# Kernel optimization log

Hardware: AMD Instinct MI355X
Metric: run time of the kernel (lower is better)

## Reference

```python
import jax, jax.numpy as jnp
import numpy as np

C = 1024
H = 16
EPS = 1e-5

def _layernorm(x, g, b):
    mu = jnp.mean(x, axis=-1, keepdims=True)
    var = jnp.mean(jnp.square(x - mu), axis=-1, keepdims=True)
    return (x - mu) * jax.lax.rsqrt(var + EPS) * g + b

def _mha(xq, xkv, wq, bq, wk, bk, wv, bv, wo, bo, causal):
    B, T, Cm = xq.shape
    Tc = xkv.shape[1]
    d = Cm // H
    q = (xq @ wq + bq).reshape(B, T, H, d)
    k = (xkv @ wk + bk).reshape(B, Tc, H, d)
    v = (xkv @ wv + bv).reshape(B, Tc, H, d)
    att = jnp.einsum('bthd,bshd->bhts', q, k) * (1.0 / np.sqrt(d))
    if causal:
        mask = jnp.tril(jnp.ones((T, Tc), dtype=bool))
        att = jnp.where(mask[None, None], att, -jnp.inf)
    att = jax.nn.softmax(att, axis=-1)
    y = jnp.einsum('bhts,bshd->bthd', att, v).reshape(B, T, Cm)
    return y @ wo + bo


def setup_inputs() -> dict:
    key = jax.random.key(0)
    ks = jax.random.split(key, 20)
    s = 0.02
    w = lambda k: (s * jax.random.normal(k, (C, C))).astype(jnp.float32)
    inp = {
        'x': jax.random.normal(ks[0], (4, 1024, C), dtype=jnp.float32),
        'context': jax.random.normal(ks[1], (4, 1024, C), dtype=jnp.float32),
        'ln1_g': jnp.ones((C,)), 'ln1_b': jnp.zeros((C,)),
        'ln2_g': jnp.ones((C,)), 'ln2_b': jnp.zeros((C,)),
        'sa_wq': w(ks[2]), 'sa_bq': jnp.zeros((C,)),
        'sa_wk': w(ks[3]), 'sa_bk': jnp.zeros((C,)),
        'sa_wv': w(ks[4]), 'sa_bv': jnp.zeros((C,)),
        'sa_wo': w(ks[5]), 'sa_bo': jnp.zeros((C,)),
        'ca_wq': w(ks[6]), 'ca_bq': jnp.zeros((C,)),
        'ca_wk': w(ks[7]), 'ca_bk': jnp.zeros((C,)),
        'ca_wv': w(ks[8]), 'ca_bv': jnp.zeros((C,)),
        'ca_wo': w(ks[9]), 'ca_bo': jnp.zeros((C,)),
        'mlp_w1': (s * jax.random.normal(ks[10], (C, 4 * C))).astype(jnp.float32),
        'mlp_b1': jnp.zeros((4 * C,)),
        'mlp_w2': (s * jax.random.normal(ks[11], (4 * C, C))).astype(jnp.float32),
        'mlp_b2': jnp.zeros((C,)),
    }
    return inp


def reference(x, context, ln1_g, ln1_b, ln2_g, ln2_b,
              sa_wq, sa_bq, sa_wk, sa_bk, sa_wv, sa_bv, sa_wo, sa_bo,
              ca_wq, ca_bq, ca_wk, ca_bk, ca_wv, ca_bv, ca_wo, ca_bo,
              mlp_w1, mlp_b1, mlp_w2, mlp_b2):
    # x = x + self_attn(ln1(x))  (causal)
    x = x + _mha(_layernorm(x, ln1_g, ln1_b), _layernorm(x, ln1_g, ln1_b),
                 sa_wq, sa_bq, sa_wk, sa_bk, sa_wv, sa_bv, sa_wo, sa_bo, causal=True)
    # x = x + cross_attn(ln2(x), context)  (non-causal)
    x = x + _mha(_layernorm(x, ln2_g, ln2_b), context,
                 ca_wq, ca_bq, ca_wk, ca_bk, ca_wv, ca_bv, ca_wo, ca_bo, causal=False)
    # x = x + mlp(ln2(x))  -- note: the module reuses ln2 here (as in source)
    h = _layernorm(x, ln2_g, ln2_b)
    h = jax.nn.gelu(h @ mlp_w1 + mlp_b1, approximate=False) @ mlp_w2 + mlp_b2
    x = x + h
    return x
```

## Files before the change

### kernel.cpp

```cpp
#include <hip/hip_runtime.h>
#include <hip/hip_bf16.h>

typedef __attribute__((ext_vector_type(8))) short s8v;
typedef __attribute__((ext_vector_type(4))) float f4v;

#define DEV static __device__ __forceinline__

DEV unsigned short f2bf(float f) {
    unsigned int u = __builtin_bit_cast(unsigned int, f);
    unsigned int r = u + 0x7FFFu + ((u >> 16) & 1u);
    return (unsigned short)(r >> 16);
}

DEV f4v fzero() { f4v v = {0.f, 0.f, 0.f, 0.f}; return v; }

DEV float fgelu(float x) {
    float z = x * (1.5957691f + 0.07135482f * x * x);
    float s = __builtin_amdgcn_rcpf(1.0f + __expf(-z));
    return x * s;
}

DEV void gload16(const void* g, void* l) {
    __builtin_amdgcn_global_load_lds(
        (const __attribute__((address_space(1))) unsigned int*)g,
        (__attribute__((address_space(3))) unsigned int*)l, 16, 0, 0);
}

struct P8 { const float* p[8]; };
__global__ __launch_bounds__(256) void k_transpose8(
        P8 ws8, unsigned short* __restrict__ base) {
    __shared__ float tile[32][33];
    int z = blockIdx.z;
    const float* W = ws8.p[z];
    unsigned short* Wt = base + (size_t)z * 1024 * 1024;
    int tx = threadIdx.x & 31, ty = threadIdx.x >> 5;
    int n0 = blockIdx.x * 32, k0 = blockIdx.y * 32;
#pragma unroll
    for (int r = 0; r < 32; r += 8)
        tile[ty + r][tx] = W[(size_t)(k0 + ty + r) * 1024 + n0 + tx];
    __syncthreads();
#pragma unroll
    for (int r = 0; r < 32; r += 8)
        Wt[(size_t)(n0 + ty + r) * 1024 + k0 + tx] = f2bf(tile[tx][ty + r]);
}

__global__ __launch_bounds__(256) void k_transpose_bf16(
        const float* __restrict__ W, unsigned short* __restrict__ Wt, int K, int N) {
    __shared__ float tile[32][33];
    int tx = threadIdx.x & 31, ty = threadIdx.x >> 5;
    int n0 = blockIdx.x * 32, k0 = blockIdx.y * 32;
#pragma unroll
    for (int r = 0; r < 32; r += 8)
        tile[ty + r][tx] = W[(size_t)(k0 + ty + r) * N + n0 + tx];
    __syncthreads();
#pragma unroll
    for (int r = 0; r < 32; r += 8)
        Wt[(size_t)(n0 + ty + r) * K + k0 + tx] = f2bf(tile[tx][ty + r]);
}

__global__ __launch_bounds__(256) void k_f32_to_bf16(
        const float* __restrict__ in, unsigned short* __restrict__ out, int n) {
    int i = (blockIdx.x * 256 + threadIdx.x) * 8;
    if (i >= n) return;
    float4 a = *(const float4*)(in + i);
    float4 b = *(const float4*)(in + i + 4);
    uint4 o;
    o.x = f2bf(a.x) | ((unsigned)f2bf(a.y) << 16);
    o.y = f2bf(a.z) | ((unsigned)f2bf(a.w) << 16);
    o.z = f2bf(b.x) | ((unsigned)f2bf(b.y) << 16);
    o.w = f2bf(b.z) | ((unsigned)f2bf(b.w) << 16);
    *(uint4*)(out + i) = o;
}

__global__ __launch_bounds__(256) void k_bias_cat(
        const float* q, const float* k, const float* v,
        const float* k2, const float* v2, float* out) {
    int i = blockIdx.x * 256 + threadIdx.x;
    float val;
    if (i < 1024) val = q[i];
    else if (i < 2048) val = k[i - 1024];
    else if (i < 3072) val = v[i - 2048];
    else if (i < 4096) val = k2[i - 3072];
    else val = v2[i - 4096];
    out[i] = val;
}

__global__ __launch_bounds__(256) void k_layernorm(
        const float* __restrict__ x, const float* __restrict__ g,
        const float* __restrict__ b, unsigned short* __restrict__ out) {
    int row = blockIdx.x;
    int t = threadIdx.x;
    const float* xr = x + (size_t)row * 1024;
    float4 v = *(const float4*)(xr + t * 4);
    float s = v.x + v.y + v.z + v.w;
    float ss = v.x * v.x + v.y * v.y + v.z * v.z + v.w * v.w;
#pragma unroll
    for (int m = 1; m < 64; m <<= 1) { s += __shfl_xor(s, m); ss += __shfl_xor(ss, m); }
    __shared__ float red[16];
    int w = t >> 6;
    if ((t & 63) == 0) { red[w] = s; red[8 + w] = ss; }
    __syncthreads();
    s = red[0] + red[1] + red[2] + red[3];
    ss = red[8] + red[9] + red[10] + red[11];
    float mu = s * (1.f / 1024.f);
    float rstd = rsqrtf(ss * (1.f / 1024.f) - mu * mu + 1e-5f);
    float4 gv = *(const float4*)(g + t * 4);
    float4 bv = *(const float4*)(b + t * 4);
    float y0 = (v.x - mu) * rstd * gv.x + bv.x;
    float y1 = (v.y - mu) * rstd * gv.y + bv.y;
    float y2 = (v.z - mu) * rstd * gv.z + bv.z;
    float y3 = (v.w - mu) * rstd * gv.w + bv.w;
    uint2 o;
    o.x = f2bf(y0) | ((unsigned)f2bf(y1) << 16);
    o.y = f2bf(y2) | ((unsigned)f2bf(y3) << 16);
    *(uint2*)(out + (size_t)row * 1024 + t * 4) = o;
}

template <int EPI, int BM>
__global__ __launch_bounds__(256) void k_gemm(
        const unsigned short* __restrict__ A, const unsigned short* __restrict__ Bt,
        const float* __restrict__ bias, const float* __restrict__ res,
        void* __restrict__ outv, int M, int N, int K) {
    constexpr int WI = (BM == 128) ? 4 : 2;
    constexpr int ABUF = BM * 64;
    constexpr int BUFSZ = ABUF + 8192;
    __shared__ __align__(16) char smem[3 * BUFSZ];
    int nbx = N >> 7;
    int bid = blockIdx.x;
    int cpx = gridDim.x >> 3;
    int swz = (bid & 7) * cpx + (bid >> 3);
    int bx = swz % nbx, by = swz / nbx;
    int m0 = by * BM, n0 = bx << 7;
    int tid = threadIdx.x, w = tid >> 6, l = tid & 63;
    int wr = w >> 1, wc = w & 1;
    int lq = l >> 4, lc = l & 15;
    f4v acc[WI][4];
#pragma unroll
    for (int i = 0; i < WI; ++i)
#pragma unroll
        for (int j = 0; j < 4; ++j) acc[i][j] = fzero();
    const unsigned short* Ab = A + (size_t)m0 * K;
    const unsigned short* Bb = Bt + (size_t)n0 * K;
    int arow = w * 16 + (l >> 2);
    int ach = (((l & 3) ^ ((arow >> 1) & 3)) << 3);

    auto STAGE = [&](int t) {
        int kt = t << 5;
        char* buf = smem + (t % 3) * BUFSZ;
        gload16(Ab + (size_t)arow * K + kt + ach, buf + w * 1024);
        if constexpr (BM == 128)
            gload16(Ab + (size_t)(64 + arow) * K + kt + ach, buf + 4096 + w * 1024);
        gload16(Bb + (size_t)arow * K + kt + ach, buf + ABUF + w * 1024);
        gload16(Bb + (size_t)(64 + arow) * K + kt + ach, buf + ABUF + 4096 + w * 1024);
    };
    int cs = ((lq ^ ((lc >> 1) & 3)) << 4);
    auto COMPUTE = [&](int t) {
        const char* buf = smem + (t % 3) * BUFSZ;
        s8v af[WI], bfr[4];
#pragma unroll
        for (int i = 0; i < WI; ++i)
            af[i] = *(const s8v*)(buf + (wr * (BM / 2) + i * 16 + lc) * 64 + cs);
#pragma unroll
        for (int j = 0; j < 4; ++j)
            bfr[j] = *(const s8v*)(buf + ABUF + (wc * 64 + j * 16 + lc) * 64 + cs);
#pragma unroll
        for (int i = 0; i < WI; ++i)
#pragma unroll
            for (int j = 0; j < 4; ++j)
                acc[i][j] = __builtin_amdgcn_mfma_f32_16x16x32_bf16(af[i], bfr[j], acc[i][j], 0, 0, 0);
    };

    int NT = K >> 5;
    STAGE(0); STAGE(1);
    if constexpr (BM == 128) asm volatile("s_waitcnt vmcnt(4)" ::: "memory");
    else                     asm volatile("s_waitcnt vmcnt(3)" ::: "memory");
    __builtin_amdgcn_s_barrier();
    for (int t = 0; t < NT; ++t) {
        if (t + 2 < NT) STAGE(t + 2);
        COMPUTE(t);
        if (t + 2 < NT) {
            if constexpr (BM == 128) asm volatile("s_waitcnt vmcnt(4)" ::: "memory");
            else                     asm volatile("s_waitcnt vmcnt(3)" ::: "memory");
        } else if (t + 1 < NT) {
            asm volatile("s_waitcnt vmcnt(0)" ::: "memory");
        }
        __builtin_amdgcn_s_barrier();
    }

    float* esc = (float*)smem + w * 1088;
#pragma unroll
    for (int i = 0; i < WI; ++i) {
#pragma unroll
        for (int j = 0; j < 4; ++j)
#pragma unroll
            for (int r = 0; r < 4; ++r)
                esc[(lq * 4 + r) * 68 + j * 16 + lc] = acc[i][j][r];
#pragma unroll
        for (int p = 0; p < 4; ++p) {
            int rr = p * 4 + lq;
            float4 v = *(const float4*)(esc + rr * 68 + lc * 4);
            int row = m0 + wr * (BM / 2) + i * 16 + rr;
            int col = n0 + wc * 64 + lc * 4;
            float4 bv = *(const float4*)(bias + col);
            v.x += bv.x; v.y += bv.y; v.z += bv.z; v.w += bv.w;
            size_t idx = (size_t)row * N + col;
            if (EPI == 0) {
                ushort4 o;
                o.x = f2bf(v.x); o.y = f2bf(v.y); o.z = f2bf(v.z); o.w = f2bf(v.w);
                *(ushort4*)((unsigned short*)outv + idx) = o;
            } else if (EPI == 1) {
                ushort4 o;
                o.x = f2bf(fgelu(v.x)); o.y = f2bf(fgelu(v.y));
                o.z = f2bf(fgelu(v.z)); o.w = f2bf(fgelu(v.w));
                *(ushort4*)((unsigned short*)outv + idx) = o;
            } else {
                float4 rv = *(const float4*)(res + idx);
                v.x += rv.x; v.y += rv.y; v.z += rv.z; v.w += rv.w;
                *(float4*)((float*)outv + idx) = v;
            }
        }
    }
}

template <bool CAUSAL>
__global__ __launch_bounds__(256) void k_attn(
        const unsigned short* __restrict__ Q, int ldq,
        const unsigned short* __restrict__ Kp, int ldk,
        const unsigned short* __restrict__ Vp, int ldv,
        unsigned short* __restrict__ O, int ldo, int T) {
    __shared__ unsigned short Ks[64 * 64];
    __shared__ unsigned short Vt[64 * 64];
    __shared__ unsigned short Ps[4][16 * 64];
    int nqt = T >> 6;
    int qt0, qt1, bh;
    if (CAUSAL) {
        int pairs = nqt >> 1;
        int pr = blockIdx.x % pairs;
        bh = blockIdx.x / pairs;
        qt0 = pr; qt1 = nqt - 1 - pr;
    } else {
        qt1 = blockIdx.x % nqt;
        bh = blockIdx.x / nqt;
        qt0 = 0;
    }
    int b = bh >> 4, h = bh & 15;
    int tid = threadIdx.x, w = tid >> 6, l = tid & 63;
    int lq = l >> 4, lc = l & 15;
    size_t qoff = (size_t)b * T * ldq + h * 64;
    size_t koff = (size_t)b * T * ldk + h * 64;
    size_t voff = (size_t)b * T * ldv + h * 64;
    s8v qf1[2], qf0[2];
    {
        const unsigned short* qp = Q + qoff + (size_t)(qt1 * 64 + w * 16 + lc) * ldq + lq * 8;
        qf1[0] = *(const s8v*)qp;
        qf1[1] = *(const s8v*)(qp + 32);
        if (CAUSAL) {
            const unsigned short* q0p = Q + qoff + (size_t)(qt0 * 64 + w * 16 + lc) * ldq + lq * 8;
            qf0[0] = *(const s8v*)q0p;
            qf0[1] = *(const s8v*)(q0p + 32);
        }
    }
    s8v ones;
#pragma unroll
    for (int i = 0; i < 8; ++i) ones[i] = (short)0x3F80;
    f4v o1[4], o0[4];
    float m1r[4], l1r[4], m0r[4], l0r[4];
#pragma unroll
    for (int j = 0; j < 4; ++j) {
        o1[j] = fzero(); o0[j] = fzero();
        m1r[j] = -3.0e38f; l1r[j] = 0.f; m0r[j] = -3.0e38f; l0r[j] = 0.f;
    }
    int p = tid & 31, dbase = (tid >> 5) * 8;

    auto SMPV = [&](f4v (&sa)[4], f4v (&oa)[4], float (&mr)[4], float (&lr)[4],
                    int qt, int kt) {
        bool diag = CAUSAL && kt == qt;
#pragma unroll
        for (int j = 0; j < 4; ++j) {
            float pv[4];
            float tm = -3.0e38f;
#pragma unroll
            for (int jn = 0; jn < 4; ++jn) {
                float sv = sa[jn][j] * 0.125f;
                if (diag) {
                    int qg = w * 16 + lq * 4 + j;
                    int kg = jn * 16 + lc;
                    if (kg > qg) sv = -3.0e38f;
                }
                pv[jn] = sv;
                tm = fmaxf(tm, sv);
            }
#pragma unroll
            for (int m = 1; m < 16; m <<= 1) tm = fmaxf(tm, __shfl_xor(tm, m));
            float mnew = fmaxf(mr[j], tm);
            float alpha = __expf(mr[j] - mnew);
            mr[j] = mnew;
#pragma unroll
            for (int jn = 0; jn < 4; ++jn) {
                float e = __expf(pv[jn] - mnew);
                int colx = jn * 16 + lc, rowx = lq * 4 + j;
                *(unsigned short*)((char*)Ps[w] + rowx * 128 +
                                   ((((colx >> 3) ^ (rowx & 7)) << 4) | ((colx & 7) << 1))) = f2bf(e);
            }
            lr[j] *= alpha;
#pragma unroll
            for (int jn = 0; jn < 4; ++jn) oa[jn][j] *= alpha;
        }
        f4v sone = fzero();
#pragma unroll
        for (int kc = 0; kc < 2; ++kc) {
            s8v af = *(const s8v*)((const char*)Ps[w] + lc * 128 +
                                   (((kc * 4 + lq) ^ (lc & 7)) << 4));
            sone = __builtin_amdgcn_mfma_f32_16x16x32_bf16(af, ones, sone, 0, 0, 0);
#pragma unroll
            for (int jn = 0; jn < 4; ++jn) {
                int dd = jn * 16 + lc;
                s8v bf = *(const s8v*)((const char*)Vt + dd * 128 +
                                       (((kc * 4 + lq) ^ (dd & 7)) << 4));
                oa[jn] = __builtin_amdgcn_mfma_f32_16x16x32_bf16(af, bf, oa[jn], 0, 0, 0);
            }
        }
#pragma unroll
        for (int j = 0; j < 4; ++j) lr[j] += sone[j];
    };

    int ktend = CAUSAL ? (qt1 + 1) : nqt;
    for (int kt = 0; kt < ktend; ++kt) {
#pragma unroll
        for (int s = 0; s < 2; ++s) {
            int idx = s * 256 + w * 64 + l;
            int t = idx >> 3;
            int ch = (idx & 7) ^ (t & 7);
            gload16(Kp + koff + (size_t)(kt * 64 + t) * ldk + ch * 8,
                    (char*)Ks + s * 4096 + w * 1024);
        }
        {
            const unsigned short* vp = Vp + voff + (size_t)(kt * 64 + 2 * p) * ldv + dbase;
            s8v v0 = *(const s8v*)vp;
            s8v v1 = *(const s8v*)(vp + ldv);
#pragma unroll
            for (int j = 0; j < 8; ++j) {
                int dd = dbase + j;
                unsigned int val = (unsigned short)v0[j] | ((unsigned)(unsigned short)v1[j] << 16);
                *(unsigned int*)((char*)Vt + dd * 128 +
                                 ((((p >> 2) ^ (dd & 7)) << 4) | ((p & 3) << 2))) = val;
            }
        }
        __syncthreads();
        bool do0 = CAUSAL && (kt <= qt0);
        f4v sa1[4], sa0[4];
#pragma unroll
        for (int jn = 0; jn < 4; ++jn) {
            sa1[jn] = fzero();
            int t = jn * 16 + lc;
#pragma unroll
            for (int kc = 0; kc < 2; ++kc) {
                s8v bf = *(const s8v*)((const char*)Ks + t * 128 +
                                       (((kc * 4 + lq) ^ (t & 7)) << 4));
                sa1[jn] = __builtin_amdgcn_mfma_f32_16x16x32_bf16(qf1[kc], bf, sa1[jn], 0, 0, 0);
            }
        }
        if (do0) {
#pragma unroll
            for (int jn = 0; jn < 4; ++jn) {
                sa0[jn] = fzero();
                int t = jn * 16 + lc;
#pragma unroll
                for (int kc = 0; kc < 2; ++kc) {
                    s8v bf = *(const s8v*)((const char*)Ks + t * 128 +
                                           (((kc * 4 + lq) ^ (t & 7)) << 4));
                    sa0[jn] = __builtin_amdgcn_mfma_f32_16x16x32_bf16(qf0[kc], bf, sa0[jn], 0, 0, 0);
                }
            }
        }
        SMPV(sa1, o1, m1r, l1r, qt1, kt);
        if (do0) SMPV(sa0, o0, m0r, l0r, qt0, kt);
        __syncthreads();
    }
#pragma unroll
    for (int j = 0; j < 4; ++j) {
        float inv = 1.0f / l1r[j];
        int row = qt1 * 64 + w * 16 + lq * 4 + j;
#pragma unroll
        for (int jn = 0; jn < 4; ++jn)
            O[(size_t)(b * T + row) * ldo + h * 64 + jn * 16 + lc] = f2bf(o1[jn][j] * inv);
    }
    if (CAUSAL) {
#pragma unroll
        for (int j = 0; j < 4; ++j) {
            float inv = 1.0f / l0r[j];
            int row = qt0 * 64 + w * 16 + lq * 4 + j;
#pragma unroll
            for (int jn = 0; jn < 4; ++jn)
                O[(size_t)(b * T + row) * ldo + h * 64 + jn * 16 + lc] = f2bf(o0[jn][j] * inv);
        }
    }
}

extern "C" void kernel_launch(void* const* d_in, const int* in_sizes, int n_in,
                              void* d_out, int out_size, void* d_ws, size_t ws_size,
                              hipStream_t stream) {
    const float* x     = (const float*)d_in[0];
    const float* ctx   = (const float*)d_in[1];
    const float* ln1_g = (const float*)d_in[2];
    const float* ln1_b = (const float*)d_in[3];
    const float* ln2_g = (const float*)d_in[4];
    const float* ln2_b = (const float*)d_in[5];
    const float* sa_wq = (const float*)d_in[6];  const float* sa_bq = (const float*)d_in[7];
    const float* sa_wk = (const float*)d_in[8];  const float* sa_bk = (const float*)d_in[9];
    const float* sa_wv = (const float*)d_in[10]; const float* sa_bv = (const float*)d_in[11];
    const float* sa_wo = (const float*)d_in[12]; const float* sa_bo = (const float*)d_in[13];
    const float* ca_wq = (const float*)d_in[14]; const float* ca_bq = (const float*)d_in[15];
    const float* ca_wk = (const float*)d_in[16]; const float* ca_bk = (const float*)d_in[17];
    const float* ca_wv = (const float*)d_in[18]; const float* ca_bv = (const float*)d_in[19];
    const float* ca_wo = (const float*)d_in[20]; const float* ca_bo = (const float*)d_in[21];
    const float* w1 = (const float*)d_in[22]; const float* b1 = (const float*)d_in[23];
    const float* w2 = (const float*)d_in[24]; const float* b2 = (const float*)d_in[25];
    float* out = (float*)d_out;

    char* ws = (char*)d_ws;
    const size_t MB = 1024 * 1024;
    unsigned short* wt_base = (unsigned short*)(ws + 0 * MB);
    unsigned short* wt_saq = wt_base + 0 * 1024 * 1024;
    unsigned short* wt_cak = wt_base + 5 * 1024 * 1024;
    unsigned short* wt_sao = wt_base + 3 * 1024 * 1024;
    unsigned short* wt_caq = wt_base + 4 * 1024 * 1024;
    unsigned short* wt_cao = wt_base + 7 * 1024 * 1024;
    unsigned short* w1t    = (unsigned short*)(ws + 16 * MB);
    unsigned short* w2t    = (unsigned short*)(ws + 24 * MB);
    unsigned short* ctxb   = (unsigned short*)(ws + 32 * MB);
    float*          x1     = (float*)        (ws + 40 * MB);
    unsigned short* qbuf   = (unsigned short*)(ws + 56 * MB);
    unsigned short* kbuf   = (unsigned short*)(ws + 64 * MB);
    unsigned short* hln    = (unsigned short*)(ws + 80 * MB);
    float*          bcat   = (float*)        (ws + 88 * MB);
    unsigned short* qkv = qbuf;
    unsigned short* kv  = kbuf;
    unsigned short* m1  = qbuf;
    unsigned short* h3  = ctxb;

    dim3 blk(256);
    P8 ws8;
    ws8.p[0] = sa_wq; ws8.p[1] = sa_wk; ws8.p[2] = sa_wv; ws8.p[3] = sa_wo;
    ws8.p[4] = ca_wq; ws8.p[5] = ca_wk; ws8.p[6] = ca_wv; ws8.p[7] = ca_wo;
    k_transpose8<<<dim3(32, 32, 8), blk, 0, stream>>>(ws8, wt_base);
    k_transpose_bf16<<<dim3(128, 32), blk, 0, stream>>>(w1, w1t, 1024, 4096);
    k_transpose_bf16<<<dim3(32, 128), blk, 0, stream>>>(w2, w2t, 4096, 1024);
    k_f32_to_bf16<<<dim3(2048), blk, 0, stream>>>(ctx, ctxb, 4 * 1024 * 1024);
    k_bias_cat<<<dim3(20), blk, 0, stream>>>(sa_bq, sa_bk, sa_bv, ca_bk, ca_bv, bcat);

    k_layernorm<<<dim3(4096), blk, 0, stream>>>(x, ln1_g, ln1_b, hln);
    k_gemm<0, 128><<<dim3(24 * 32), blk, 0, stream>>>(hln, wt_saq, bcat, nullptr, qkv, 4096, 3072, 1024);
    k_attn<true><<<dim3(512), blk, 0, stream>>>(qkv, 3072, qkv + 1024, 3072, qkv + 2048, 3072,
                                                hln, 1024, 1024);
    k_gemm<2, 64><<<dim3(64 * 8), blk, 0, stream>>>(hln, wt_sao, sa_bo, x, x1, 4096, 1024, 1024);

    k_layernorm<<<dim3(4096), blk, 0, stream>>>(x1, ln2_g, ln2_b, hln);
    k_gemm<0, 64><<<dim3(64 * 8), blk, 0, stream>>>(hln, wt_caq, ca_bq, nullptr, qbuf, 4096, 1024, 1024);
    k_gemm<0, 128><<<dim3(16 * 32), blk, 0, stream>>>(ctxb, wt_cak, bcat + 3072, nullptr, kv, 4096, 2048, 1024);
    k_attn<false><<<dim3(1024), blk, 0, stream>>>(qbuf, 1024, kv, 2048, kv + 1024, 2048,
                                                  hln, 1024, 1024);
    k_gemm<2, 64><<<dim3(64 * 8), blk, 0, stream>>>(hln, wt_cao, ca_bo, x1, out, 4096, 1024, 1024);

    k_layernorm<<<dim3(4096), blk, 0, stream>>>(out, ln2_g, ln2_b, h3);
    k_gemm<1, 128><<<dim3(32 * 32), blk, 0, stream>>>(h3, w1t, b1, nullptr, m1, 4096, 4096, 1024);
    k_gemm<2, 64><<<dim3(64 * 8), blk, 0, stream>>>(m1, w2t, b2, out, out, 4096, 1024, 4096);
}
```

Baseline: 359.9 us.

## Double-buffer K/V tiles in attention and transpose S for per-lane softmax

The attention kernel now double-buffers K and V in shared memory, prefetching the next key tile while the current one is processed, which removes one barrier per iteration and hides global load latency. The QK^T MFMA operands are swapped so each lane holds a full query row's scores, letting the row max be computed with two shuffles instead of four per row, and softmax uses exp2 with a folded log2e scale. This doubles the K/V LDS footprint, which may reduce occupancy, and the extra prefetched V registers raise register pressure.

```diff
diff --git a/kernel.cpp b/kernel.cpp
--- a/kernel.cpp
+++ b/kernel.cpp
@@ -228,8 +228,8 @@
         const unsigned short* __restrict__ Kp, int ldk,
         const unsigned short* __restrict__ Vp, int ldv,
         unsigned short* __restrict__ O, int ldo, int T) {
-    __shared__ unsigned short Ks[64 * 64];
-    __shared__ unsigned short Vt[64 * 64];
+    __shared__ unsigned short Ks[2][64 * 64];
+    __shared__ unsigned short Vt[2][64 * 64];
     __shared__ unsigned short Ps[4][16 * 64];
     int nqt = T >> 6;
     int qt0, qt1, bh;
@@ -264,118 +264,133 @@
 #pragma unroll
     for (int i = 0; i < 8; ++i) ones[i] = (short)0x3F80;
     f4v o1[4], o0[4];
-    float m1r[4], l1r[4], m0r[4], l0r[4];
+    float l1r[4], l0r[4];
+    float m1 = -3.0e38f, m0 = -3.0e38f;
 #pragma unroll
     for (int j = 0; j < 4; ++j) {
-        o1[j] = fzero(); o0[j] = fzero();
-        m1r[j] = -3.0e38f; l1r[j] = 0.f; m0r[j] = -3.0e38f; l0r[j] = 0.f;
+        o1[j] = fzero(); o0[j] = fzero(); l1r[j] = 0.f; l0r[j] = 0.f;
     }
     int p = tid & 31, dbase = (tid >> 5) * 8;
-
-    auto SMPV = [&](f4v (&sa)[4], f4v (&oa)[4], float (&mr)[4], float (&lr)[4],
-                    int qt, int kt) {
-        bool diag = CAUSAL && kt == qt;
-#pragma unroll
-        for (int j = 0; j < 4; ++j) {
-            float pv[4];
-            float tm = -3.0e38f;
-#pragma unroll
-            for (int jn = 0; jn < 4; ++jn) {
-                float sv = sa[jn][j] * 0.125f;
-                if (diag) {
-                    int qg = w * 16 + lq * 4 + j;
-                    int kg = jn * 16 + lc;
-                    if (kg > qg) sv = -3.0e38f;
-                }
-                pv[jn] = sv;
-                tm = fmaxf(tm, sv);
-            }
-#pragma unroll
-            for (int m = 1; m < 16; m <<= 1) tm = fmaxf(tm, __shfl_xor(tm, m));
-            float mnew = fmaxf(mr[j], tm);
-            float alpha = __expf(mr[j] - mnew);
-            mr[j] = mnew;
-#pragma unroll
-            for (int jn = 0; jn < 4; ++jn) {
-                float e = __expf(pv[jn] - mnew);
-                int colx = jn * 16 + lc, rowx = lq * 4 + j;
-                *(unsigned short*)((char*)Ps[w] + rowx * 128 +
-                                   ((((colx >> 3) ^ (rowx & 7)) << 4) | ((colx & 7) << 1))) = f2bf(e);
-            }
-            lr[j] *= alpha;
-#pragma unroll
-            for (int jn = 0; jn < 4; ++jn) oa[jn][j] *= alpha;
-        }
-        f4v sone = fzero();
-#pragma unroll
-        for (int kc = 0; kc < 2; ++kc) {
-            s8v af = *(const s8v*)((const char*)Ps[w] + lc * 128 +
-                                   (((kc * 4 + lq) ^ (lc & 7)) << 4));
-            sone = __builtin_amdgcn_mfma_f32_16x16x32_bf16(af, ones, sone, 0, 0, 0);
-#pragma unroll
-            for (int jn = 0; jn < 4; ++jn) {
-                int dd = jn * 16 + lc;
-                s8v bf = *(const s8v*)((const char*)Vt + dd * 128 +
-                                       (((kc * 4 + lq) ^ (dd & 7)) << 4));
-                oa[jn] = __builtin_amdgcn_mfma_f32_16x16x32_bf16(af, bf, oa[jn], 0, 0, 0);
-            }
-        }
-#pragma unroll
-        for (int j = 0; j < 4; ++j) lr[j] += sone[j];
-    };
-
-    int ktend = CAUSAL ? (qt1 + 1) : nqt;
-    for (int kt = 0; kt < ktend; ++kt) {
+    s8v v0r, v1r;
+
+    auto STAGE_K = [&](int kt, int bufi) {
 #pragma unroll
         for (int s = 0; s < 2; ++s) {
             int idx = s * 256 + w * 64 + l;
             int t = idx >> 3;
             int ch = (idx & 7) ^ (t & 7);
             gload16(Kp + koff + (size_t)(kt * 64 + t) * ldk + ch * 8,
-                    (char*)Ks + s * 4096 + w * 1024);
-        }
-        {
-            const unsigned short* vp = Vp + voff + (size_t)(kt * 64 + 2 * p) * ldv + dbase;
-            s8v v0 = *(const s8v*)vp;
-            s8v v1 = *(const s8v*)(vp + ldv);
-#pragma unroll
-            for (int j = 0; j < 8; ++j) {
-                int dd = dbase + j;
-                unsigned int val = (unsigned short)v0[j] | ((unsigned)(unsigned short)v1[j] << 16);
-                *(unsigned int*)((char*)Vt + dd * 128 +
-                                 ((((p >> 2) ^ (dd & 7)) << 4) | ((p & 3) << 2))) = val;
+                    (char*)Ks[bufi] + s * 4096 + w * 1024);
+        }
+    };
+    auto LOAD_V = [&](int kt) {
+        const unsigned short* vp = Vp + voff + (size_t)(kt * 64 + 2 * p) * ldv + dbase;
+        v0r = *(const s8v*)vp;
+        v1r = *(const s8v*)(vp + ldv);
+    };
+    auto WRITE_V = [&](int bufi) {
+#pragma unroll
+        for (int j = 0; j < 8; ++j) {
+            int dd = dbase + j;
+            unsigned int val = (unsigned short)v0r[j] | ((unsigned)(unsigned short)v1r[j] << 16);
+            *(unsigned int*)((char*)Vt[bufi] + dd * 128 +
+                             ((((p >> 2) ^ (dd & 7)) << 4) | ((p & 3) << 2))) = val;
+        }
+    };
+
+    const float SC = 0.18033688011112042f;
+
+    auto SMPV = [&](f4v (&sa)[4], f4v (&oa)[4], float& mr, float (&lr)[4],
+                    int bufi, int qt, int kt) {
+        bool diag = CAUSAL && (kt == qt);
+        int qloc = w * 16 + lc;
+        float pv[16];
+        float tm = -3.0e38f;
+#pragma unroll
+        for (int jn = 0; jn < 4; ++jn)
+#pragma unroll
+            for (int j = 0; j < 4; ++j) {
+                float sv = sa[jn][j] * SC;
+                if (diag && (jn * 16 + lq * 4 + j > qloc)) sv = -3.0e38f;
+                pv[jn * 4 + j] = sv;
+                tm = fmaxf(tm, sv);
             }
-        }
-        __syncthreads();
+        tm = fmaxf(tm, __shfl_xor(tm, 16));
+        tm = fmaxf(tm, __shfl_xor(tm, 32));
+        float mnew = fmaxf(mr, tm);
+        float alpha = exp2f(mr - mnew);
+        mr = mnew;
+#pragma unroll
+        for (int j = 0; j < 4; ++j) {
+            float aj = __shfl(alpha, lq * 4 + j);
+            lr[j] *= aj;
+#pragma unroll
+            for (int jn = 0; jn < 4; ++jn) oa[jn][j] *= aj;
+        }
+#pragma unroll
+        for (int jn = 0; jn < 4; ++jn) {
+            int chunk = (jn * 2 + (lq >> 1)) ^ (lc & 7);
+            char* basep = (char*)Ps[w] + lc * 128 + (chunk << 4) + ((lq & 1) << 3);
+            unsigned e01 = f2bf(exp2f(pv[jn * 4 + 0] - mnew)) |
+                           ((unsigned)f2bf(exp2f(pv[jn * 4 + 1] - mnew)) << 16);
+            unsigned e23 = f2bf(exp2f(pv[jn * 4 + 2] - mnew)) |
+                           ((unsigned)f2bf(exp2f(pv[jn * 4 + 3] - mnew)) << 16);
+            *(unsigned*)basep = e01;
+            *(unsigned*)(basep + 4) = e23;
+        }
+        s8v pa[2];
+#pragma unroll
+        for (int kc = 0; kc < 2; ++kc)
+            pa[kc] = *(const s8v*)((const char*)Ps[w] + lc * 128 +
+                                   (((kc * 4 + lq) ^ (lc & 7)) << 4));
+        f4v sone = fzero();
+#pragma unroll
+        for (int kc = 0; kc < 2; ++kc) {
+            sone = __builtin_amdgcn_mfma_f32_16x16x32_bf16(pa[kc], ones, sone, 0, 0, 0);
+#pragma unroll
+            for (int jn = 0; jn < 4; ++jn) {
+                int dd = jn * 16 + lc;
+                s8v bf = *(const s8v*)((const char*)Vt[bufi] + dd * 128 +
+                                       (((kc * 4 + lq) ^ (dd & 7)) << 4));
+                oa[jn] = __builtin_amdgcn_mfma_f32_16x16x32_bf16(pa[kc], bf, oa[jn], 0, 0, 0);
+            }
+        }
+#pragma unroll
+        for (int j = 0; j < 4; ++j) lr[j] += sone[j];
+    };
+
+    int ktend = CAUSAL ? (qt1 + 1) : nqt;
+    STAGE_K(0, 0); LOAD_V(0);
+    asm volatile("s_waitcnt vmcnt(0)" ::: "memory");
+    WRITE_V(0);
+    __syncthreads();
+    int buf = 0;
+    for (int kt = 0; kt < ktend; ++kt) {
+        bool pf = (kt + 1 < ktend);
+        if (pf) { STAGE_K(kt + 1, buf ^ 1); LOAD_V(kt + 1); }
         bool do0 = CAUSAL && (kt <= qt0);
         f4v sa1[4], sa0[4];
 #pragma unroll
         for (int jn = 0; jn < 4; ++jn) {
-            sa1[jn] = fzero();
+            sa1[jn] = fzero(); sa0[jn] = fzero();
             int t = jn * 16 + lc;
 #pragma unroll
             for (int kc = 0; kc < 2; ++kc) {
-                s8v bf = *(const s8v*)((const char*)Ks + t * 128 +
+                s8v kf = *(const s8v*)((const char*)Ks[buf] + t * 128 +
                                        (((kc * 4 + lq) ^ (t & 7)) << 4));
-                sa1[jn] = __builtin_amdgcn_mfma_f32_16x16x32_bf16(qf1[kc], bf, sa1[jn], 0, 0, 0);
+                sa1[jn] = __builtin_amdgcn_mfma_f32_16x16x32_bf16(kf, qf1[kc], sa1[jn], 0, 0, 0);
+                if (do0)
+                    sa0[jn] = __builtin_amdgcn_mfma_f32_16x16x32_bf16(kf, qf0[kc], sa0[jn], 0, 0, 0);
             }
         }
-        if (do0) {
-#pragma unroll
-            for (int jn = 0; jn < 4; ++jn) {
-                sa0[jn] = fzero();
-                int t = jn * 16 + lc;
-#pragma unroll
-                for (int kc = 0; kc < 2; ++kc) {
-                    s8v bf = *(const s8v*)((const char*)Ks + t * 128 +
-                                           (((kc * 4 + lq) ^ (t & 7)) << 4));
-                    sa0[jn] = __builtin_amdgcn_mfma_f32_16x16x32_bf16(qf0[kc], bf, sa0[jn], 0, 0, 0);
-                }
-            }
-        }
-        SMPV(sa1, o1, m1r, l1r, qt1, kt);
-        if (do0) SMPV(sa0, o0, m0r, l0r, qt0, kt);
+        SMPV(sa1, o1, m1, l1r, buf, qt1, kt);
+        if (do0) SMPV(sa0, o0, m0, l0r, buf, qt0, kt);
+        if (pf) {
+            asm volatile("s_waitcnt vmcnt(0)" ::: "memory");
+            WRITE_V(buf ^ 1);
+        }
         __syncthreads();
+        buf ^= 1;
     }
 #pragma unroll
     for (int j = 0; j < 4; ++j) {
```

Result: faster. 352.8 us (-2.0%).
